# Performance work log

Hardware: AMD Instinct MI355X
Metric: run time of the kernel (lower is better)

Reference implementation:

```python
import jax, jax.numpy as jnp
import numpy as np

B, S, H, NH = 2, 2048, 1024, 16
HD = H // NH  # 64


def setup_inputs() -> dict:
    key = jax.random.key(0)
    ks = jax.random.split(key, 9)
    w = lambda k: jax.random.normal(k, (H, H), dtype=jnp.float32) * 0.02  # torch Linear weight [out,in]
    b = lambda k: jax.random.normal(k, (H,), dtype=jnp.float32) * 0.02
    return {
        "hidden_states": jax.random.normal(ks[0], (B, S, H), dtype=jnp.float32),
        "Wq": w(ks[1]), "bq": b(ks[2]),
        "Wk": w(ks[3]), "bk": b(ks[4]),
        "Wv": w(ks[5]), "bv": b(ks[6]),
        "Wo": w(ks[7]), "bo": b(ks[8]),
    }


def reference(hidden_states, Wq, bq, Wk, bk, Wv, bv, Wo, bo):
    b, s, h = hidden_states.shape
    nh, hd = NH, h // NH

    def proj(W, bias):
        y = hidden_states @ W.T + bias  # torch Linear: x W^T + b
        return y.reshape(b, s, nh, hd).transpose(0, 2, 1, 3)  # [b, h, s, d]

    q = proj(Wq, bq)
    k = proj(Wk, bk)
    v = proj(Wv, bv)

    scale = jnp.sqrt(jnp.asarray(hd, dtype=q.dtype))
    scores = jnp.einsum("bhqd,bhkd->bhqk", q, k) / scale  # [b, h, s, s]
    pos = jnp.arange(s)
    causal = pos[:, None] < pos[None, :]  # True where masked (key after query)
    scores = jnp.where(causal[None, None], -jnp.inf, scores)
    attn = jax.nn.softmax(scores, axis=-1)
    out = jnp.einsum("bhqk,bhkd->bhqd", attn, v)
    out = out.transpose(0, 2, 1, 3).reshape(b, s, h)
    return out @ Wo.T + bo
```

## Files before the change

kernel.cpp:

```cpp
#include <hip/hip_runtime.h>
#include <stdint.h>

typedef __bf16 bf16;
typedef __attribute__((ext_vector_type(2))) __bf16 bf16x2;
typedef __attribute__((ext_vector_type(4))) __bf16 bf16x4;
typedef __attribute__((ext_vector_type(8))) __bf16 bf16x8;
typedef __attribute__((ext_vector_type(4))) float f32x4;

#define B_  2
#define S_  2048
#define H_  1024
#define NH_ 16
#define HD_ 64
#define ST  72
#define STV 136

__device__ __forceinline__ void glds16(const bf16* g, bf16* l) {
  __builtin_amdgcn_global_load_lds(
      (const __attribute__((address_space(1))) uint32_t*)g,
      (__attribute__((address_space(3))) uint32_t*)l, 16, 0, 0);
}

__global__ __launch_bounds__(256) void cvt_f32_bf16(
    const float* __restrict__ s0, bf16* __restrict__ d0, int n0,
    const float* __restrict__ s1, bf16* __restrict__ d1,
    const float* __restrict__ s2, bf16* __restrict__ d2,
    const float* __restrict__ s3, bf16* __restrict__ d3,
    const float* __restrict__ s4, bf16* __restrict__ d4, int nw)
{
  const float* s; bf16* d; int n;
  switch (blockIdx.y) {
    case 0:  s = s0; d = d0; n = n0; break;
    case 1:  s = s1; d = d1; n = nw; break;
    case 2:  s = s2; d = d2; n = nw; break;
    case 3:  s = s3; d = d3; n = nw; break;
    default: s = s4; d = d4; n = nw; break;
  }
  const int i = (blockIdx.x * 256 + threadIdx.x) * 8;
  if (i >= n) return;
  float4 v0 = *(const float4*)(s + i);
  float4 v1 = *(const float4*)(s + i + 4);
  bf16x8 o;
  o[0] = (bf16)v0.x; o[1] = (bf16)v0.y; o[2] = (bf16)v0.z; o[3] = (bf16)v0.w;
  o[4] = (bf16)v1.x; o[5] = (bf16)v1.y; o[6] = (bf16)v1.z; o[7] = (bf16)v1.w;
  *(bf16x8*)(d + i) = o;
}

template <typename TY>
__global__ __launch_bounds__(256) void gemm_bt_bias(
    const bf16* __restrict__ X,
    const bf16* __restrict__ W0, const bf16* __restrict__ W1, const bf16* __restrict__ W2,
    const float* __restrict__ b0, const float* __restrict__ b1, const float* __restrict__ b2,
    TY* __restrict__ Y0, TY* __restrict__ Y1, TY* __restrict__ Y2,
    int M, int N, int K)
{
  const bf16* W; const float* bias; TY* Y;
  if (blockIdx.z == 0)      { W = W0; bias = b0; Y = Y0; }
  else if (blockIdx.z == 1) { W = W1; bias = b1; Y = Y1; }
  else                      { W = W2; bias = b2; Y = Y2; }

  __shared__ __align__(16) bf16 As[2][128 * 32];
  __shared__ __align__(16) bf16 Bs[2][128 * 32];

  const int tid  = threadIdx.x;
  const int lane = tid & 63;
  const int wave = tid >> 6;
  const int m0 = blockIdx.y * 128;
  const int n0 = blockIdx.x * 128;
  const int wm = (wave >> 1) * 64;
  const int wn = (wave & 1) * 64;

  const int r0 = tid >> 2,            c0 = (tid & 3) * 8;
  const int r1 = (256 + tid) >> 2,    c1 = ((256 + tid) & 3) * 8;
  const int cb0 = (wave * 64) * 8;
  const int cb1 = (256 + wave * 64) * 8;

  f32x4 acc[4][4] = {};

  glds16(X + (size_t)(m0 + r0) * K + c0, &As[0][cb0]);
  glds16(W + (size_t)(n0 + r0) * K + c0, &Bs[0][cb0]);
  glds16(X + (size_t)(m0 + r1) * K + c1, &As[0][cb1]);
  glds16(W + (size_t)(n0 + r1) * K + c1, &Bs[0][cb1]);

  int pb = 0;
  for (int k0 = 0; k0 < K; k0 += 32, pb ^= 1) {
    __syncthreads();

    if (k0 + 32 < K) {
      const int kn = k0 + 32;
      glds16(X + (size_t)(m0 + r0) * K + kn + c0, &As[pb ^ 1][cb0]);
      glds16(W + (size_t)(n0 + r0) * K + kn + c0, &Bs[pb ^ 1][cb0]);
      glds16(X + (size_t)(m0 + r1) * K + kn + c1, &As[pb ^ 1][cb1]);
      glds16(W + (size_t)(n0 + r1) * K + kn + c1, &Bs[pb ^ 1][cb1]);
    }

    bf16x8 a[4], b[4];
#pragma unroll
    for (int i = 0; i < 4; ++i)
      a[i] = *(const bf16x8*)&As[pb][(wm + i * 16 + (lane & 15)) * 32 + (lane >> 4) * 8];
#pragma unroll
    for (int i = 0; i < 4; ++i)
      b[i] = *(const bf16x8*)&Bs[pb][(wn + i * 16 + (lane & 15)) * 32 + (lane >> 4) * 8];
#pragma unroll
    for (int mi = 0; mi < 4; ++mi)
#pragma unroll
      for (int ni = 0; ni < 4; ++ni)
        acc[mi][ni] = __builtin_amdgcn_mfma_f32_16x16x32_bf16(a[mi], b[ni], acc[mi][ni], 0, 0, 0);
  }

#pragma unroll
  for (int mi = 0; mi < 4; ++mi) {
    const int row = m0 + wm + mi * 16 + (lane >> 4) * 4;
#pragma unroll
    for (int ni = 0; ni < 4; ++ni) {
      const int col = n0 + wn + ni * 16 + (lane & 15);
      const float bv = bias[col];
#pragma unroll
      for (int r = 0; r < 4; ++r)
        Y[(size_t)(row + r) * N + col] = (TY)(acc[mi][ni][r] + bv);
    }
  }
}

__global__ __launch_bounds__(256) void attn_causal(
    const bf16* __restrict__ Q, const bf16* __restrict__ K,
    const bf16* __restrict__ V, bf16* __restrict__ O)
{
  const int pair = blockIdx.x;
  const int bh   = blockIdx.y;
  const int b    = bh >> 4;
  const int h    = bh & 15;

  const int tid  = threadIdx.x;
  const int lane = tid & 63;
  const int wave = tid >> 6;
  const int quad = lane >> 4;
  const int l15  = lane & 15;
  const size_t headoff = (size_t)b * S_ * H_ + (size_t)h * HD_;
  const float SCL = 0.125f * 1.44269504f;

  __shared__ __align__(16) bf16 Qs[64 * ST];
  __shared__ __align__(16) bf16 Ks[128 * ST];
  __shared__ __align__(16) bf16 Vt[64 * STV];
  __shared__ __align__(16) bf16 Ps[4][16 * STV];

  for (int phase = 0; phase < 2; ++phase) {
    const int qt = phase ? (31 - pair) : pair;
    const int q0 = qt * 64;
    __syncthreads();

#pragma unroll
    for (int it = 0; it < 2; ++it) {
      const int c = it * 256 + tid, row = c >> 3, col = (c & 7) * 8;
      *(bf16x8*)&Qs[row * ST + col] =
          *(const bf16x8*)(Q + headoff + (size_t)(q0 + row) * H_ + col);
    }

    const int qrow = q0 + wave * 16 + l15;
    float mr = -1e30f, lr = 0.0f;
    f32x4 oacc[4] = {};

    const int niter = (qt >> 1) + 1;
    for (int it = 0; it < niter; ++it) {
      const int k0 = it * 128;
      __syncthreads();

#pragma unroll
      for (int j = 0; j < 4; ++j) {
        const int c = j * 256 + tid, row = c >> 3, col = (c & 7) * 8;
        *(bf16x8*)&Ks[row * ST + col] =
            *(const bf16x8*)(K + headoff + (size_t)(k0 + row) * H_ + col);
      }
      {
        const int vr = (tid & 63) * 2;
        const int vc = (tid >> 6) * 16;
        bf16x8 a0 = *(const bf16x8*)(V + headoff + (size_t)(k0 + vr) * H_ + vc);
        bf16x8 a1 = *(const bf16x8*)(V + headoff + (size_t)(k0 + vr) * H_ + vc + 8);
        bf16x8 c0 = *(const bf16x8*)(V + headoff + (size_t)(k0 + vr + 1) * H_ + vc);
        bf16x8 c1 = *(const bf16x8*)(V + headoff + (size_t)(k0 + vr + 1) * H_ + vc + 8);
#pragma unroll
        for (int e = 0; e < 8; ++e) {
          bf16x2 p0; p0[0] = a0[e]; p0[1] = c0[e];
          *(bf16x2*)&Vt[(vc + e) * STV + vr] = p0;
          bf16x2 p1; p1[0] = a1[e]; p1[1] = c1[e];
          *(bf16x2*)&Vt[(vc + 8 + e) * STV + vr] = p1;
        }
      }
      __syncthreads();

      f32x4 sacc[8] = {};
#pragma unroll
      for (int ks = 0; ks < 2; ++ks) {
        bf16x8 bq = *(const bf16x8*)&Qs[(wave * 16 + l15) * ST + ks * 32 + quad * 8];
#pragma unroll
        for (int mb = 0; mb < 8; ++mb) {
          bf16x8 ak = *(const bf16x8*)&Ks[(mb * 16 + l15) * ST + ks * 32 + quad * 8];
          sacc[mb] = __builtin_amdgcn_mfma_f32_16x16x32_bf16(ak, bq, sacc[mb], 0, 0, 0);
        }
      }

      float sv[8][4];
      if (it == niter - 1) {
#pragma unroll
        for (int mb = 0; mb < 8; ++mb) {
          const int kb = k0 + mb * 16 + quad * 4;
#pragma unroll
          for (int r = 0; r < 4; ++r) {
            const float s = sacc[mb][r] * SCL;
            sv[mb][r] = (kb + r > qrow) ? -1e30f : s;
          }
        }
      } else {
#pragma unroll
        for (int mb = 0; mb < 8; ++mb)
#pragma unroll
          for (int r = 0; r < 4; ++r)
            sv[mb][r] = sacc[mb][r] * SCL;
      }

      float mx = -1e30f;
#pragma unroll
      for (int mb = 0; mb < 8; ++mb)
        mx = fmaxf(mx, fmaxf(fmaxf(sv[mb][0], sv[mb][1]), fmaxf(sv[mb][2], sv[mb][3])));
      mx = fmaxf(mx, __shfl_xor(mx, 16, 64));
      mx = fmaxf(mx, __shfl_xor(mx, 32, 64));
      const float mnew  = fmaxf(mr, mx);
      const float alpha = __builtin_amdgcn_exp2f(mr - mnew);
      mr = mnew;

      float sum = 0.0f;
#pragma unroll
      for (int mb = 0; mb < 8; ++mb) {
        bf16x4 pw;
#pragma unroll
        for (int r = 0; r < 4; ++r) {
          const float p = __builtin_amdgcn_exp2f(sv[mb][r] - mnew);
          sum += p;
          pw[r] = (bf16)p;
        }
        *(bf16x4*)&Ps[wave][l15 * STV + mb * 16 + quad * 4] = pw;
      }
      sum += __shfl_xor(sum, 16, 64);
      sum += __shfl_xor(sum, 32, 64);
      lr = lr * alpha + sum;
#pragma unroll
      for (int mb = 0; mb < 4; ++mb)
#pragma unroll
        for (int r = 0; r < 4; ++r) oacc[mb][r] *= alpha;

#pragma unroll
      for (int ks = 0; ks < 4; ++ks) {
        bf16x8 bp = *(const bf16x8*)&Ps[wave][l15 * STV + ks * 32 + quad * 8];
#pragma unroll
        for (int mb = 0; mb < 4; ++mb) {
          bf16x8 av = *(const bf16x8*)&Vt[(mb * 16 + l15) * STV + ks * 32 + quad * 8];
          oacc[mb] = __builtin_amdgcn_mfma_f32_16x16x32_bf16(av, bp, oacc[mb], 0, 0, 0);
        }
      }
    }

    const float inv = 1.0f / lr;
#pragma unroll
    for (int mb = 0; mb < 4; ++mb) {
      bf16x4 o;
#pragma unroll
      for (int r = 0; r < 4; ++r) o[r] = (bf16)(oacc[mb][r] * inv);
      *(bf16x4*)(O + headoff + (size_t)qrow * H_ + mb * 16 + quad * 4) = o;
    }
  }
}

extern "C" void kernel_launch(void* const* d_in, const int* in_sizes, int n_in,
                              void* d_out, int out_size, void* d_ws, size_t ws_size,
                              hipStream_t stream) {
  const float* hs = (const float*)d_in[0];
  const float* Wq = (const float*)d_in[1]; const float* bq = (const float*)d_in[2];
  const float* Wk = (const float*)d_in[3]; const float* bk = (const float*)d_in[4];
  const float* Wv = (const float*)d_in[5]; const float* bv = (const float*)d_in[6];
  const float* Wo = (const float*)d_in[7]; const float* bo = (const float*)d_in[8];
  float* out = (float*)d_out;

  const size_t elems = (size_t)B_ * S_ * H_;
  const size_t wel   = (size_t)H_ * H_;
  bf16* hsb = (bf16*)d_ws;
  bf16* AO  = hsb;
  bf16* Wqb = hsb + elems;
  bf16* Wkb = Wqb + wel;
  bf16* Wvb = Wkb + wel;
  bf16* Wob = Wvb + wel;
  bf16* Qw  = Wob + wel;
  bf16* Kw  = Qw + elems;
  bf16* Vw  = Kw + elems;

  cvt_f32_bf16<<<dim3(2048, 5), dim3(256), 0, stream>>>(
      hs, hsb, (int)elems, Wq, Wqb, Wk, Wkb, Wv, Wvb, Wo, Wob, (int)wel);

  const int M = B_ * S_;
  gemm_bt_bias<bf16><<<dim3(H_ / 128, M / 128, 3), dim3(256), 0, stream>>>(
      hsb, Wqb, Wkb, Wvb, bq, bk, bv, Qw, Kw, Vw, M, H_, H_);

  attn_causal<<<dim3(16, B_ * NH_), dim3(256), 0, stream>>>(Qw, Kw, Vw, AO);

  gemm_bt_bias<float><<<dim3(H_ / 128, M / 128, 1), dim3(256), 0, stream>>>(
      AO, Wob, Wob, Wob, bo, bo, bo, out, out, out, M, H_, H_);
}
```

Before: 202.7 us.

## Keep P in registers via 16x16x16 MFMA, drop paired-tile scheduling

The attention kernel now holds Q fragments and the softmax probabilities in registers. P feeds the PV product directly through 16x16x16 bf16 MFMAs, whose register layout matches the score accumulator, so the Qs and Ps shared-memory staging and their LDS round trips go away. The grid changes from 16 paired q-tiles per block to 32 blocks with one q-tile each. The kernel also gains launch_bounds occupancy hints and s_setprio around the MFMA sections. Dropping the pairing gives up the causal load balance, so blocks now have very uneven work, and the smaller MFMA shape issues more instructions.

```diff
diff --git a/kernel.cpp b/kernel.cpp
--- a/kernel.cpp
+++ b/kernel.cpp
@@ -6,6 +6,7 @@
 typedef __attribute__((ext_vector_type(4))) __bf16 bf16x4;
 typedef __attribute__((ext_vector_type(8))) __bf16 bf16x8;
 typedef __attribute__((ext_vector_type(4))) float f32x4;
+typedef __attribute__((ext_vector_type(4))) short s16x4;
 
 #define B_  2
 #define S_  2048
@@ -19,6 +20,20 @@
   __builtin_amdgcn_global_load_lds(
       (const __attribute__((address_space(1))) uint32_t*)g,
       (__attribute__((address_space(3))) uint32_t*)l, 16, 0, 0);
+}
+
+__device__ __forceinline__ f32x4 pv_mfma(bf16x4 a, bf16x4 b, f32x4 c) {
+#if __has_builtin(__builtin_amdgcn_mfma_f32_16x16x16bf16_1k)
+  union U { bf16x4 h; s16x4 s; };
+  U ua; ua.h = a;
+  U ub; ub.h = b;
+  return __builtin_amdgcn_mfma_f32_16x16x16bf16_1k(ua.s, ub.s, c, 0, 0, 0);
+#else
+  f32x4 d;
+  asm volatile("v_mfma_f32_16x16x16_bf16 %0, %1, %2, %3\n\ts_nop 7\n\ts_nop 7"
+               : "=v"(d) : "v"(a), "v"(b), "v"(c));
+  return d;
+#endif
 }
 
 __global__ __launch_bounds__(256) void cvt_f32_bf16(
@@ -122,14 +137,14 @@
   }
 }
 
-__global__ __launch_bounds__(256) void attn_causal(
+__global__ __launch_bounds__(256, 4) void attn_causal(
     const bf16* __restrict__ Q, const bf16* __restrict__ K,
     const bf16* __restrict__ V, bf16* __restrict__ O)
 {
-  const int pair = blockIdx.x;
-  const int bh   = blockIdx.y;
-  const int b    = bh >> 4;
-  const int h    = bh & 15;
+  const int qt = blockIdx.x;
+  const int bh = blockIdx.y;
+  const int b  = bh >> 4;
+  const int h  = bh & 15;
 
   const int tid  = threadIdx.x;
   const int lane = tid & 63;
@@ -139,134 +154,126 @@
   const size_t headoff = (size_t)b * S_ * H_ + (size_t)h * HD_;
   const float SCL = 0.125f * 1.44269504f;
 
-  __shared__ __align__(16) bf16 Qs[64 * ST];
   __shared__ __align__(16) bf16 Ks[128 * ST];
   __shared__ __align__(16) bf16 Vt[64 * STV];
-  __shared__ __align__(16) bf16 Ps[4][16 * STV];
-
-  for (int phase = 0; phase < 2; ++phase) {
-    const int qt = phase ? (31 - pair) : pair;
-    const int q0 = qt * 64;
+
+  const int q0   = qt * 64;
+  const int qrow = q0 + wave * 16 + l15;
+
+  bf16x8 bq[2];
+  bq[0] = *(const bf16x8*)(Q + headoff + (size_t)qrow * H_ + quad * 8);
+  bq[1] = *(const bf16x8*)(Q + headoff + (size_t)qrow * H_ + 32 + quad * 8);
+
+  float mr = -1e30f, lr = 0.0f;
+  f32x4 oacc[4] = {};
+
+  const int niter = (qt >> 1) + 1;
+  for (int it = 0; it < niter; ++it) {
+    const int k0 = it * 128;
     __syncthreads();
 
 #pragma unroll
-    for (int it = 0; it < 2; ++it) {
-      const int c = it * 256 + tid, row = c >> 3, col = (c & 7) * 8;
-      *(bf16x8*)&Qs[row * ST + col] =
-          *(const bf16x8*)(Q + headoff + (size_t)(q0 + row) * H_ + col);
-    }
-
-    const int qrow = q0 + wave * 16 + l15;
-    float mr = -1e30f, lr = 0.0f;
-    f32x4 oacc[4] = {};
-
-    const int niter = (qt >> 1) + 1;
-    for (int it = 0; it < niter; ++it) {
-      const int k0 = it * 128;
-      __syncthreads();
-
-#pragma unroll
-      for (int j = 0; j < 4; ++j) {
-        const int c = j * 256 + tid, row = c >> 3, col = (c & 7) * 8;
-        *(bf16x8*)&Ks[row * ST + col] =
-            *(const bf16x8*)(K + headoff + (size_t)(k0 + row) * H_ + col);
-      }
-      {
-        const int vr = (tid & 63) * 2;
-        const int vc = (tid >> 6) * 16;
-        bf16x8 a0 = *(const bf16x8*)(V + headoff + (size_t)(k0 + vr) * H_ + vc);
-        bf16x8 a1 = *(const bf16x8*)(V + headoff + (size_t)(k0 + vr) * H_ + vc + 8);
-        bf16x8 c0 = *(const bf16x8*)(V + headoff + (size_t)(k0 + vr + 1) * H_ + vc);
-        bf16x8 c1 = *(const bf16x8*)(V + headoff + (size_t)(k0 + vr + 1) * H_ + vc + 8);
-#pragma unroll
-        for (int e = 0; e < 8; ++e) {
-          bf16x2 p0; p0[0] = a0[e]; p0[1] = c0[e];
-          *(bf16x2*)&Vt[(vc + e) * STV + vr] = p0;
-          bf16x2 p1; p1[0] = a1[e]; p1[1] = c1[e];
-          *(bf16x2*)&Vt[(vc + 8 + e) * STV + vr] = p1;
+    for (int j = 0; j < 4; ++j) {
+      const int c = j * 256 + tid, row = c >> 3, col = (c & 7) * 8;
+      *(bf16x8*)&Ks[row * ST + col] =
+          *(const bf16x8*)(K + headoff + (size_t)(k0 + row) * H_ + col);
+    }
+    {
+      const int vr = (tid & 63) * 2;
+      const int vc = (tid >> 6) * 16;
+      bf16x8 a0 = *(const bf16x8*)(V + headoff + (size_t)(k0 + vr) * H_ + vc);
+      bf16x8 a1 = *(const bf16x8*)(V + headoff + (size_t)(k0 + vr) * H_ + vc + 8);
+      bf16x8 c0 = *(const bf16x8*)(V + headoff + (size_t)(k0 + vr + 1) * H_ + vc);
+      bf16x8 c1 = *(const bf16x8*)(V + headoff + (size_t)(k0 + vr + 1) * H_ + vc + 8);
+#pragma unroll
+      for (int e = 0; e < 8; ++e) {
+        bf16x2 p0; p0[0] = a0[e]; p0[1] = c0[e];
+        *(bf16x2*)&Vt[(vc + e) * STV + vr] = p0;
+        bf16x2 p1; p1[0] = a1[e]; p1[1] = c1[e];
+        *(bf16x2*)&Vt[(vc + 8 + e) * STV + vr] = p1;
+      }
+    }
+    __syncthreads();
+
+    f32x4 sacc[8] = {};
+    __builtin_amdgcn_s_setprio(1);
+#pragma unroll
+    for (int ks = 0; ks < 2; ++ks) {
+#pragma unroll
+      for (int mb = 0; mb < 8; ++mb) {
+        bf16x8 ak = *(const bf16x8*)&Ks[(mb * 16 + l15) * ST + ks * 32 + quad * 8];
+        sacc[mb] = __builtin_amdgcn_mfma_f32_16x16x32_bf16(ak, bq[ks], sacc[mb], 0, 0, 0);
+      }
+    }
+    __builtin_amdgcn_s_setprio(0);
+
+    if (it == niter - 1) {
+#pragma unroll
+      for (int mb = 0; mb < 8; ++mb) {
+        const int kb = k0 + mb * 16 + quad * 4;
+#pragma unroll
+        for (int r = 0; r < 4; ++r) {
+          const float s = sacc[mb][r] * SCL;
+          sacc[mb][r] = (kb + r > qrow) ? -1e30f : s;
         }
       }
-      __syncthreads();
-
-      f32x4 sacc[8] = {};
-#pragma unroll
-      for (int ks = 0; ks < 2; ++ks) {
-        bf16x8 bq = *(const bf16x8*)&Qs[(wave * 16 + l15) * ST + ks * 32 + quad * 8];
-#pragma unroll
-        for (int mb = 0; mb < 8; ++mb) {
-          bf16x8 ak = *(const bf16x8*)&Ks[(mb * 16 + l15) * ST + ks * 32 + quad * 8];
-          sacc[mb] = __builtin_amdgcn_mfma_f32_16x16x32_bf16(ak, bq, sacc[mb], 0, 0, 0);
-        }
-      }
-
-      float sv[8][4];
-      if (it == niter - 1) {
-#pragma unroll
-        for (int mb = 0; mb < 8; ++mb) {
-          const int kb = k0 + mb * 16 + quad * 4;
-#pragma unroll
-          for (int r = 0; r < 4; ++r) {
-            const float s = sacc[mb][r] * SCL;
-            sv[mb][r] = (kb + r > qrow) ? -1e30f : s;
-          }
-        }
-      } else {
-#pragma unroll
-        for (int mb = 0; mb < 8; ++mb)
-#pragma unroll
-          for (int r = 0; r < 4; ++r)
-            sv[mb][r] = sacc[mb][r] * SCL;
-      }
-
-      float mx = -1e30f;
+    } else {
 #pragma unroll
       for (int mb = 0; mb < 8; ++mb)
-        mx = fmaxf(mx, fmaxf(fmaxf(sv[mb][0], sv[mb][1]), fmaxf(sv[mb][2], sv[mb][3])));
-      mx = fmaxf(mx, __shfl_xor(mx, 16, 64));
-      mx = fmaxf(mx, __shfl_xor(mx, 32, 64));
-      const float mnew  = fmaxf(mr, mx);
-      const float alpha = __builtin_amdgcn_exp2f(mr - mnew);
-      mr = mnew;
-
-      float sum = 0.0f;
-#pragma unroll
-      for (int mb = 0; mb < 8; ++mb) {
-        bf16x4 pw;
-#pragma unroll
-        for (int r = 0; r < 4; ++r) {
-          const float p = __builtin_amdgcn_exp2f(sv[mb][r] - mnew);
-          sum += p;
-          pw[r] = (bf16)p;
-        }
-        *(bf16x4*)&Ps[wave][l15 * STV + mb * 16 + quad * 4] = pw;
-      }
-      sum += __shfl_xor(sum, 16, 64);
-      sum += __shfl_xor(sum, 32, 64);
-      lr = lr * alpha + sum;
-#pragma unroll
-      for (int mb = 0; mb < 4; ++mb)
-#pragma unroll
-        for (int r = 0; r < 4; ++r) oacc[mb][r] *= alpha;
-
-#pragma unroll
-      for (int ks = 0; ks < 4; ++ks) {
-        bf16x8 bp = *(const bf16x8*)&Ps[wave][l15 * STV + ks * 32 + quad * 8];
-#pragma unroll
-        for (int mb = 0; mb < 4; ++mb) {
-          bf16x8 av = *(const bf16x8*)&Vt[(mb * 16 + l15) * STV + ks * 32 + quad * 8];
-          oacc[mb] = __builtin_amdgcn_mfma_f32_16x16x32_bf16(av, bp, oacc[mb], 0, 0, 0);
-        }
-      }
-    }
-
-    const float inv = 1.0f / lr;
-#pragma unroll
-    for (int mb = 0; mb < 4; ++mb) {
-      bf16x4 o;
-#pragma unroll
-      for (int r = 0; r < 4; ++r) o[r] = (bf16)(oacc[mb][r] * inv);
-      *(bf16x4*)(O + headoff + (size_t)qrow * H_ + mb * 16 + quad * 4) = o;
-    }
+#pragma unroll
+        for (int r = 0; r < 4; ++r)
+          sacc[mb][r] = sacc[mb][r] * SCL;
+    }
+
+    float mx = -1e30f;
+#pragma unroll
+    for (int mb = 0; mb < 8; ++mb)
+      mx = fmaxf(mx, fmaxf(fmaxf(sacc[mb][0], sacc[mb][1]),
+                           fmaxf(sacc[mb][2], sacc[mb][3])));
+    mx = fmaxf(mx, __shfl_xor(mx, 16, 64));
+    mx = fmaxf(mx, __shfl_xor(mx, 32, 64));
+    const float mnew  = fmaxf(mr, mx);
+    const float alpha = __builtin_amdgcn_exp2f(mr - mnew);
+    mr = mnew;
+
+    float sum = 0.0f;
+    bf16x4 pwv[8];
+#pragma unroll
+    for (int mb = 0; mb < 8; ++mb) {
+#pragma unroll
+      for (int r = 0; r < 4; ++r) {
+        const float p = __builtin_amdgcn_exp2f(sacc[mb][r] - mnew);
+        sum += p;
+        pwv[mb][r] = (bf16)p;
+      }
+    }
+    sum += __shfl_xor(sum, 16, 64);
+    sum += __shfl_xor(sum, 32, 64);
+    lr = lr * alpha + sum;
+#pragma unroll
+    for (int db = 0; db < 4; ++db)
+#pragma unroll
+      for (int r = 0; r < 4; ++r) oacc[db][r] *= alpha;
+
+    __builtin_amdgcn_s_setprio(1);
+#pragma unroll
+    for (int mb = 0; mb < 8; ++mb) {
+#pragma unroll
+      for (int db = 0; db < 4; ++db) {
+        bf16x4 av = *(const bf16x4*)&Vt[(db * 16 + l15) * STV + mb * 16 + quad * 4];
+        oacc[db] = pv_mfma(av, pwv[mb], oacc[db]);
+      }
+    }
+    __builtin_amdgcn_s_setprio(0);
+  }
+
+  const float inv = 1.0f / lr;
+#pragma unroll
+  for (int db = 0; db < 4; ++db) {
+    bf16x4 o;
+#pragma unroll
+    for (int r = 0; r < 4; ++r) o[r] = (bf16)(oacc[db][r] * inv);
+    *(bf16x4*)(O + headoff + (size_t)qrow * H_ + db * 16 + quad * 4) = o;
   }
 }
 
@@ -299,7 +306,7 @@
   gemm_bt_bias<bf16><<<dim3(H_ / 128, M / 128, 3), dim3(256), 0, stream>>>(
       hsb, Wqb, Wkb, Wvb, bq, bk, bv, Qw, Kw, Vw, M, H_, H_);
 
-  attn_causal<<<dim3(16, B_ * NH_), dim3(256), 0, stream>>>(Qw, Kw, Vw, AO);
+  attn_causal<<<dim3(32, B_ * NH_), dim3(256), 0, stream>>>(Qw, Kw, Vw, AO);
 
   gemm_bt_bias<float><<<dim3(H_ / 128, M / 128, 1), dim3(256), 0, stream>>>(
       AO, Wob, Wob, Wob, bo, bo, bo, out, out, out, M, H_, H_);
```

After: 220.9 us. 1.09x slower.
